# Optimization experiments

Measured on AMD Instinct MI355X. Metric: run time of the kernel, lower is better.

The kernel has to match this reference:

```python
import jax, jax.numpy as jnp
import numpy as np

N_NODES = 10000
N_EDGES = 320000
D = 128  # feature dim for edges, nodes, globals


def setup_inputs() -> dict:
    key = jax.random.key(0)
    ks = jax.random.split(key, 8)
    edges = jax.random.normal(ks[0], (N_EDGES, D), dtype=jnp.float32)
    nodes = jax.random.normal(ks[1], (N_NODES, D), dtype=jnp.float32)
    globals_ = jax.random.normal(ks[2], (D,), dtype=jnp.float32)
    receivers = jax.random.randint(ks[3], (N_EDGES,), 0, N_NODES, dtype=jnp.int32).astype(jnp.int64)
    senders = jax.random.randint(ks[4], (N_EDGES,), 0, N_NODES, dtype=jnp.int32).astype(jnp.int64)
    W1 = jax.random.normal(ks[5], (4 * D, 256), dtype=jnp.float32) * (1.0 / np.sqrt(4 * D))
    b1 = jnp.zeros((256,), dtype=jnp.float32)
    W2 = jax.random.normal(ks[6], (256, D), dtype=jnp.float32) * (1.0 / np.sqrt(256))
    b2 = jnp.zeros((D,), dtype=jnp.float32)
    return {"edges": edges, "nodes": nodes, "globals_": globals_,
            "receivers": receivers, "senders": senders,
            "W1": W1, "b1": b1, "W2": W2, "b2": b2}


def reference(edges, nodes, globals_, receivers, senders, W1, b1, W2, b2):
    # Gather adjacent node features to edges, broadcast globals, concat.
    recv_feats = nodes[receivers]                 # [E, D]
    send_feats = nodes[senders]                   # [E, D]
    glob_feats = jnp.broadcast_to(globals_, (edges.shape[0], globals_.shape[0]))  # [E, D]
    x = jnp.concatenate([edges, recv_feats, send_feats, glob_feats], axis=-1)     # [E, 4D]
    # Edge-update MLP: 4D -> 256 -> D with relu.
    h = jax.nn.relu(x @ W1 + b1)
    new_edges = h @ W2 + b2                       # [E, D]
    return new_edges
```

## Files before the change

kernel.cpp:

```cpp
#include <hip/hip_runtime.h>
#include <hip/hip_bf16.h>

#define D 128
#define NH 256
#define K1 384
#define BM 64
#define E_TOTAL 320000
#define NNODES 10000

typedef __attribute__((ext_vector_type(8))) short bf16x8;
typedef __attribute__((ext_vector_type(4))) float f32x4;

__device__ __forceinline__ unsigned short f2b(float f) {
  unsigned int u = __builtin_bit_cast(unsigned int, f);
  u += 0x7fffu + ((u >> 16) & 1u);
  return (unsigned short)(u >> 16);
}

__global__ void cast_nodes_kernel(const float* __restrict__ nodes,
                                  ushort* __restrict__ out) {
  int i = (blockIdx.x * 256 + threadIdx.x) * 4;
  float4 v = *(const float4*)(nodes + i);
  ushort4 b;
  b.x = f2b(v.x); b.y = f2b(v.y); b.z = f2b(v.z); b.w = f2b(v.w);
  *(ushort4*)(out + i) = b;
}

__global__ void pack_w1_kernel(const float* __restrict__ W1,
                               ushort* __restrict__ W1p) {
  int c = blockIdx.x * 256 + threadIdx.x;
  int nt = c / (12 * 64);
  int rem = c % (12 * 64);
  int ks = rem >> 6;
  int l = rem & 63;
  int col = nt * 16 + (l & 15);
  int k0 = ks * 32 + (l >> 4) * 8;
  ushort* dst = W1p + (size_t)c * 8;
  #pragma unroll
  for (int j = 0; j < 8; ++j)
    dst[j] = f2b(W1[(size_t)(k0 + j) * NH + col]);
}

__global__ void pack_w2_kernel(const float* __restrict__ W2,
                               ushort* __restrict__ W2p) {
  int c = blockIdx.x * 256 + threadIdx.x;
  int nt2 = c / (8 * 64);
  int rem = c % (8 * 64);
  int ks = rem >> 6;
  int l = rem & 63;
  int col = nt2 * 16 + (l & 15);
  int k0 = ks * 32 + (l >> 4) * 8;
  ushort* dst = W2p + (size_t)c * 8;
  #pragma unroll
  for (int j = 0; j < 8; ++j)
    dst[j] = f2b(W2[(size_t)(k0 + j) * D + col]);
}

__global__ void cvec_kernel(const float* __restrict__ W1,
                            const float* __restrict__ b1,
                            const float* __restrict__ g,
                            float* __restrict__ cvec) {
  int n = threadIdx.x;
  float acc = b1[n];
  for (int k = 0; k < D; ++k)
    acc += g[k] * W1[(size_t)(K1 + k) * NH + n];
  cvec[n] = acc;
}

__global__ __launch_bounds__(512, 6) void fused_kernel(
    const float* __restrict__ edges,
    const ushort* __restrict__ nodes_b,
    const int* __restrict__ receivers,
    const int* __restrict__ senders,
    const ushort* __restrict__ W1p,
    const float* __restrict__ cvec,
    const ushort* __restrict__ W2p,
    const float* __restrict__ b2,
    float* __restrict__ out) {
  __shared__ char Xs[BM * 768];
  char* Hs = Xs;

  const int ebase = blockIdx.x * BM;
  const int tid = threadIdx.x;

  const int gr0 = tid >> 4;
  const int gr1 = gr0 + 32;
  const int gc = (tid & 15) << 3;
  int idx_r0 = receivers[ebase + gr0];
  int idx_r1 = receivers[ebase + gr1];
  int idx_s0 = senders[ebase + gr0];
  int idx_s1 = senders[ebase + gr1];

  float4 ev[4];
  int er[4], ec[4];
  #pragma unroll
  for (int it = 0; it < 4; ++it) {
    int ch = tid + it * 512;
    er[it] = ch >> 5;
    ec[it] = (ch & 31) << 2;
    ev[it] = *(const float4*)(edges + (size_t)(ebase + er[it]) * D + ec[it]);
  }

  uint4 gv[4];
  gv[0] = *(const uint4*)(nodes_b + (size_t)idx_r0 * D + gc);
  gv[1] = *(const uint4*)(nodes_b + (size_t)idx_r1 * D + gc);
  gv[2] = *(const uint4*)(nodes_b + (size_t)idx_s0 * D + gc);
  gv[3] = *(const uint4*)(nodes_b + (size_t)idx_s1 * D + gc);

  #pragma unroll
  for (int it = 0; it < 4; ++it) {
    ushort4 b;
    b.x = f2b(ev[it].x); b.y = f2b(ev[it].y); b.z = f2b(ev[it].z); b.w = f2b(ev[it].w);
    *(ushort4*)(Xs + er[it] * 768 + ((ec[it] * 2) ^ ((er[it] & 7) << 4))) = b;
  }
  {
    int cR = (D + gc) * 2, cS = (2 * D + gc) * 2;
    *(uint4*)(Xs + gr0 * 768 + (cR ^ ((gr0 & 7) << 4))) = gv[0];
    *(uint4*)(Xs + gr1 * 768 + (cR ^ ((gr1 & 7) << 4))) = gv[1];
    *(uint4*)(Xs + gr0 * 768 + (cS ^ ((gr0 & 7) << 4))) = gv[2];
    *(uint4*)(Xs + gr1 * 768 + (cS ^ ((gr1 & 7) << 4))) = gv[3];
  }
  __syncthreads();

  const int lane = tid & 63;
  const int wave = tid >> 6;
  const int lr = lane & 15;
  const int kg = lane >> 4;
  const int wm3 = wave >> 1;
  const int wn3 = wave & 1;

  const ushort* w1base = W1p + (size_t)(wave * 2) * 12 * 512 + lane * 8;

  f32x4 acc[2][4] = {};
  bf16x8 aw[2][2];
  #pragma unroll
  for (int ht = 0; ht < 2; ++ht)
    aw[0][ht] = *(const bf16x8*)(w1base + (size_t)ht * 12 * 512);

  #pragma unroll
  for (int ks = 0; ks < 12; ++ks) {
    const int cur = ks & 1, nxt = cur ^ 1;
    if (ks < 11) {
      #pragma unroll
      for (int ht = 0; ht < 2; ++ht)
        aw[nxt][ht] = *(const bf16x8*)(w1base + (size_t)ht * 12 * 512 + (ks + 1) * 512);
    }
    const int k0 = ks * 32 + kg * 8;
    bf16x8 xb[4];
    #pragma unroll
    for (int et = 0; et < 4; ++et) {
      int row = et * 16 + lr;
      xb[et] = *(const bf16x8*)(Xs + row * 768 + ((k0 * 2) ^ ((row & 7) << 4)));
    }
    #pragma unroll
    for (int ht = 0; ht < 2; ++ht)
      #pragma unroll
      for (int et = 0; et < 4; ++et)
        acc[ht][et] = __builtin_amdgcn_mfma_f32_16x16x32_bf16(aw[cur][ht], xb[et], acc[ht][et], 0, 0, 0);
  }

  const ushort* w2base = W2p + (size_t)(wm3 * 2) * 8 * 512 + lane * 8;
  bf16x8 aw2[2][2];
  #pragma unroll
  for (int mt = 0; mt < 2; ++mt)
    aw2[0][mt] = *(const bf16x8*)(w2base + (size_t)mt * 8 * 512);
  float4 cva = *(const float4*)(cvec + wave * 32 + kg * 4);
  float4 cvb = *(const float4*)(cvec + wave * 32 + 16 + kg * 4);

  __syncthreads();

  #pragma unroll
  for (int ht = 0; ht < 2; ++ht) {
    const float4 cvq = ht ? cvb : cva;
    const int h0b = (wave * 32 + ht * 16 + kg * 4) * 2;
    #pragma unroll
    for (int et = 0; et < 4; ++et) {
      int e = et * 16 + lr;
      float v0 = acc[ht][et][0] + cvq.x;
      float v1 = acc[ht][et][1] + cvq.y;
      float v2 = acc[ht][et][2] + cvq.z;
      float v3 = acc[ht][et][3] + cvq.w;
      v0 = v0 > 0.f ? v0 : 0.f;
      v1 = v1 > 0.f ? v1 : 0.f;
      v2 = v2 > 0.f ? v2 : 0.f;
      v3 = v3 > 0.f ? v3 : 0.f;
      uint2 pk;
      pk.x = (unsigned)f2b(v0) | ((unsigned)f2b(v1) << 16);
      pk.y = (unsigned)f2b(v2) | ((unsigned)f2b(v3) << 16);
      *(uint2*)(Hs + e * 512 + (h0b ^ ((e & 7) << 4))) = pk;
    }
  }
  __syncthreads();

  float4 ba = *(const float4*)(b2 + wm3 * 32 + kg * 4);
  float4 bb2 = *(const float4*)(b2 + wm3 * 32 + 16 + kg * 4);
  f32x4 acc2[2][2] = {};
  #pragma unroll
  for (int ks = 0; ks < 8; ++ks) {
    const int cur = ks & 1, nxt = cur ^ 1;
    if (ks < 7) {
      #pragma unroll
      for (int mt = 0; mt < 2; ++mt)
        aw2[nxt][mt] = *(const bf16x8*)(w2base + (size_t)mt * 8 * 512 + (ks + 1) * 512);
    }
    const int k0 = ks * 32 + kg * 8;
    bf16x8 hb[2];
    #pragma unroll
    for (int et2 = 0; et2 < 2; ++et2) {
      int e = wn3 * 32 + et2 * 16 + lr;
      hb[et2] = *(const bf16x8*)(Hs + e * 512 + ((k0 * 2) ^ ((e & 7) << 4)));
    }
    #pragma unroll
    for (int mt = 0; mt < 2; ++mt)
      #pragma unroll
      for (int et2 = 0; et2 < 2; ++et2)
        acc2[mt][et2] = __builtin_amdgcn_mfma_f32_16x16x32_bf16(aw2[cur][mt], hb[et2], acc2[mt][et2], 0, 0, 0);
  }

  #pragma unroll
  for (int mt = 0; mt < 2; ++mt) {
    const float4 bq = mt ? bb2 : ba;
    const int c0 = wm3 * 32 + mt * 16 + kg * 4;
    #pragma unroll
    for (int et2 = 0; et2 < 2; ++et2) {
      int e = wn3 * 32 + et2 * 16 + lr;
      float4 o;
      o.x = acc2[mt][et2][0] + bq.x;
      o.y = acc2[mt][et2][1] + bq.y;
      o.z = acc2[mt][et2][2] + bq.z;
      o.w = acc2[mt][et2][3] + bq.w;
      *(float4*)(out + (size_t)(ebase + e) * D + c0) = o;
    }
  }
}

extern "C" void kernel_launch(void* const* d_in, const int* in_sizes, int n_in,
                              void* d_out, int out_size, void* d_ws, size_t ws_size,
                              hipStream_t stream) {
  const float* edges     = (const float*)d_in[0];
  const float* nodes     = (const float*)d_in[1];
  const float* globals_  = (const float*)d_in[2];
  const int*   receivers = (const int*)d_in[3];
  const int*   senders   = (const int*)d_in[4];
  const float* W1        = (const float*)d_in[5];
  const float* b1        = (const float*)d_in[6];
  const float* W2        = (const float*)d_in[7];
  const float* b2        = (const float*)d_in[8];
  float* out = (float*)d_out;

  char* ws = (char*)d_ws;
  ushort* nodes_b = (ushort*)ws;
  ushort* W1p     = (ushort*)(ws + 2560000);
  ushort* W2p     = (ushort*)(ws + 2560000 + 196608);
  float*  cvec    = (float*)(ws + 2560000 + 196608 + 65536);

  hipLaunchKernelGGL(cast_nodes_kernel, dim3(NNODES * D / 1024), dim3(256), 0, stream,
                     nodes, nodes_b);
  hipLaunchKernelGGL(pack_w1_kernel, dim3(48), dim3(256), 0, stream, W1, W1p);
  hipLaunchKernelGGL(pack_w2_kernel, dim3(16), dim3(256), 0, stream, W2, W2p);
  hipLaunchKernelGGL(cvec_kernel, dim3(1), dim3(256), 0, stream,
                     W1, b1, globals_, cvec);
  hipLaunchKernelGGL(fused_kernel, dim3(E_TOTAL / BM), dim3(512), 0, stream,
                     edges, nodes_b, receivers, senders, W1p, cvec, W2p, b2, out);
}
```

Before: 151.8 us.

## Precompute per-node first-layer projections and gather them instead of node features

Splits the first linear layer by linearity: node features are projected once per node through the receiver and sender slices of W1 into bf16 tables. The edge kernel gathers these 256-wide projections and adds them, plus the globals bias, into the hidden pre-activation. This cuts the edge GEMM K dimension from 384 to 128 and removes the node cast kernel. The cost is gathering 256-wide bf16 rows instead of 128-wide ones, extra bf16 rounding of the summed projections, a new pre-kernel, and lower declared occupancy.

```diff
diff --git a/kernel.cpp b/kernel.cpp
--- a/kernel.cpp
+++ b/kernel.cpp
@@ -3,7 +3,6 @@
 
 #define D 128
 #define NH 256
-#define K1 384
 #define BM 64
 #define E_TOTAL 320000
 #define NNODES 10000
@@ -16,26 +15,34 @@
   u += 0x7fffu + ((u >> 16) & 1u);
   return (unsigned short)(u >> 16);
 }
-
-__global__ void cast_nodes_kernel(const float* __restrict__ nodes,
-                                  ushort* __restrict__ out) {
-  int i = (blockIdx.x * 256 + threadIdx.x) * 4;
-  float4 v = *(const float4*)(nodes + i);
-  ushort4 b;
-  b.x = f2b(v.x); b.y = f2b(v.y); b.z = f2b(v.z); b.w = f2b(v.w);
-  *(ushort4*)(out + i) = b;
+__device__ __forceinline__ unsigned pk2(float a, float b) {
+  return (unsigned)f2b(a) | ((unsigned)f2b(b) << 16);
+}
+__device__ __forceinline__ uint4 pack8(float4 a, float4 b) {
+  uint4 r;
+  r.x = pk2(a.x, a.y); r.y = pk2(a.z, a.w);
+  r.z = pk2(b.x, b.y); r.w = pk2(b.z, b.w);
+  return r;
+}
+__device__ __forceinline__ float lo2f(unsigned u) {
+  return __builtin_bit_cast(float, u << 16);
+}
+__device__ __forceinline__ float hi2f(unsigned u) {
+  return __builtin_bit_cast(float, u & 0xffff0000u);
 }
 
 __global__ void pack_w1_kernel(const float* __restrict__ W1,
-                               ushort* __restrict__ W1p) {
+                               ushort* __restrict__ W1pk) {
   int c = blockIdx.x * 256 + threadIdx.x;
-  int nt = c / (12 * 64);
-  int rem = c % (12 * 64);
-  int ks = rem >> 6;
-  int l = rem & 63;
+  int s = c >> 12;
+  int rem = c & 4095;
+  int nt = rem >> 8;
+  int rem2 = rem & 255;
+  int ks = rem2 >> 6;
+  int l = rem2 & 63;
   int col = nt * 16 + (l & 15);
-  int k0 = ks * 32 + (l >> 4) * 8;
-  ushort* dst = W1p + (size_t)c * 8;
+  int k0 = s * 128 + ks * 32 + (l >> 4) * 8;
+  ushort* dst = W1pk + (size_t)c * 8;
   #pragma unroll
   for (int j = 0; j < 8; ++j)
     dst[j] = f2b(W1[(size_t)(k0 + j) * NH + col]);
@@ -63,62 +70,156 @@
   int n = threadIdx.x;
   float acc = b1[n];
   for (int k = 0; k < D; ++k)
-    acc += g[k] * W1[(size_t)(K1 + k) * NH + n];
+    acc += g[k] * W1[(size_t)(384 + k) * NH + n];
   cvec[n] = acc;
 }
 
-__global__ __launch_bounds__(512, 6) void fused_kernel(
+__global__ __launch_bounds__(512, 4) void nodeh_kernel(
+    const float* __restrict__ nodes,
+    const ushort* __restrict__ W1pk,
+    ushort* __restrict__ tblR,
+    ushort* __restrict__ tblS) {
+  __shared__ char Xn[BM * 256];
+  const int role = blockIdx.y;
+  ushort* __restrict__ tbl = role ? tblS : tblR;
+  const int nb = blockIdx.x * BM;
+  const int tid = threadIdx.x;
+
+  {
+    int row = tid >> 4;
+    int cc = (tid & 15) * 16;
+    #pragma unroll
+    for (int q = 0; q < 2; ++q) {
+      int r = row + q * 32;
+      int rg = nb + r; if (rg >= NNODES) rg = NNODES - 1;
+      const float* np = nodes + (size_t)rg * D + (tid & 15) * 8;
+      float4 u0 = *(const float4*)np;
+      float4 u1 = *(const float4*)(np + 4);
+      *(uint4*)(Xn + r * 256 + (cc ^ ((r & 7) << 4))) = pack8(u0, u1);
+    }
+  }
+  __syncthreads();
+
+  const int lane = tid & 63;
+  const int wave = tid >> 6;
+  const int lr = lane & 15;
+  const int kg = lane >> 4;
+
+  const ushort* wb = W1pk + (size_t)(1 + role) * 32768
+                   + (size_t)(wave * 2) * 2048 + lane * 8;
+  f32x4 acc[2][4] = {};
+  bf16x8 aw[2][2];
+  #pragma unroll
+  for (int ht = 0; ht < 2; ++ht)
+    aw[0][ht] = *(const bf16x8*)(wb + ht * 2048);
+
+  #pragma unroll
+  for (int ks = 0; ks < 4; ++ks) {
+    const int cur = ks & 1, nxt = cur ^ 1;
+    if (ks < 3) {
+      #pragma unroll
+      for (int ht = 0; ht < 2; ++ht)
+        aw[nxt][ht] = *(const bf16x8*)(wb + ht * 2048 + (ks + 1) * 512);
+    }
+    const int k0 = ks * 32 + kg * 8;
+    bf16x8 xb[4];
+    #pragma unroll
+    for (int et = 0; et < 4; ++et) {
+      int row = et * 16 + lr;
+      xb[et] = *(const bf16x8*)(Xn + row * 256 + ((k0 * 2) ^ ((row & 7) << 4)));
+    }
+    #pragma unroll
+    for (int ht = 0; ht < 2; ++ht)
+      #pragma unroll
+      for (int et = 0; et < 4; ++et)
+        acc[ht][et] = __builtin_amdgcn_mfma_f32_16x16x32_bf16(aw[cur][ht], xb[et], acc[ht][et], 0, 0, 0);
+  }
+
+  #pragma unroll
+  for (int ht = 0; ht < 2; ++ht) {
+    int h0 = wave * 32 + ht * 16 + kg * 4;
+    #pragma unroll
+    for (int et = 0; et < 4; ++et) {
+      int n = nb + et * 16 + lr;
+      if (n < NNODES) {
+        uint2 pk;
+        pk.x = pk2(acc[ht][et][0], acc[ht][et][1]);
+        pk.y = pk2(acc[ht][et][2], acc[ht][et][3]);
+        *(uint2*)(tbl + (size_t)n * NH + h0) = pk;
+      }
+    }
+  }
+}
+
+__global__ __launch_bounds__(512, 4) void fused_kernel(
     const float* __restrict__ edges,
-    const ushort* __restrict__ nodes_b,
     const int* __restrict__ receivers,
     const int* __restrict__ senders,
-    const ushort* __restrict__ W1p,
+    const ushort* __restrict__ W1pk,
+    const ushort* __restrict__ tblR,
+    const ushort* __restrict__ tblS,
     const float* __restrict__ cvec,
     const ushort* __restrict__ W2p,
     const float* __restrict__ b2,
     float* __restrict__ out) {
-  __shared__ char Xs[BM * 768];
-  char* Hs = Xs;
+  __shared__ char Xs[BM * 256];
+  __shared__ char Hp[BM * 512];
 
   const int ebase = blockIdx.x * BM;
   const int tid = threadIdx.x;
 
-  const int gr0 = tid >> 4;
-  const int gr1 = gr0 + 32;
-  const int gc = (tid & 15) << 3;
-  int idx_r0 = receivers[ebase + gr0];
-  int idx_r1 = receivers[ebase + gr1];
-  int idx_s0 = senders[ebase + gr0];
-  int idx_s1 = senders[ebase + gr1];
-
-  float4 ev[4];
-  int er[4], ec[4];
-  #pragma unroll
-  for (int it = 0; it < 4; ++it) {
-    int ch = tid + it * 512;
-    er[it] = ch >> 5;
-    ec[it] = (ch & 31) << 2;
-    ev[it] = *(const float4*)(edges + (size_t)(ebase + er[it]) * D + ec[it]);
-  }
-
-  uint4 gv[4];
-  gv[0] = *(const uint4*)(nodes_b + (size_t)idx_r0 * D + gc);
-  gv[1] = *(const uint4*)(nodes_b + (size_t)idx_r1 * D + gc);
-  gv[2] = *(const uint4*)(nodes_b + (size_t)idx_s0 * D + gc);
-  gv[3] = *(const uint4*)(nodes_b + (size_t)idx_s1 * D + gc);
-
-  #pragma unroll
-  for (int it = 0; it < 4; ++it) {
-    ushort4 b;
-    b.x = f2b(ev[it].x); b.y = f2b(ev[it].y); b.z = f2b(ev[it].z); b.w = f2b(ev[it].w);
-    *(ushort4*)(Xs + er[it] * 768 + ((ec[it] * 2) ^ ((er[it] & 7) << 4))) = b;
-  }
+  const int ge = tid >> 5;
+  const int gc0 = (tid & 31) * 8;
+  int idxR[4], idxS[4];
+  #pragma unroll
+  for (int j = 0; j < 4; ++j) {
+    idxR[j] = receivers[ebase + ge + j * 16];
+    idxS[j] = senders[ebase + ge + j * 16];
+  }
+
+  const int erow = tid >> 4;
+  const int ecc = (tid & 15) * 16;
+  float4 e0, e1, e2, e3;
   {
-    int cR = (D + gc) * 2, cS = (2 * D + gc) * 2;
-    *(uint4*)(Xs + gr0 * 768 + (cR ^ ((gr0 & 7) << 4))) = gv[0];
-    *(uint4*)(Xs + gr1 * 768 + (cR ^ ((gr1 & 7) << 4))) = gv[1];
-    *(uint4*)(Xs + gr0 * 768 + (cS ^ ((gr0 & 7) << 4))) = gv[2];
-    *(uint4*)(Xs + gr1 * 768 + (cS ^ ((gr1 & 7) << 4))) = gv[3];
+    const float* ep0 = edges + (size_t)(ebase + erow) * D + (tid & 15) * 8;
+    e0 = *(const float4*)ep0;
+    e1 = *(const float4*)(ep0 + 4);
+    const float* ep1 = edges + (size_t)(ebase + erow + 32) * D + (tid & 15) * 8;
+    e2 = *(const float4*)ep1;
+    e3 = *(const float4*)(ep1 + 4);
+  }
+
+  float4 cva = *(const float4*)(cvec + gc0);
+  float4 cvb = *(const float4*)(cvec + gc0 + 4);
+
+  uint4 gR[4], gS[4];
+  #pragma unroll
+  for (int j = 0; j < 4; ++j) {
+    gR[j] = *(const uint4*)(tblR + (size_t)idxR[j] * NH + gc0);
+    gS[j] = *(const uint4*)(tblS + (size_t)idxS[j] * NH + gc0);
+  }
+
+  *(uint4*)(Xs + erow * 256 + (ecc ^ ((erow & 7) << 4))) = pack8(e0, e1);
+  {
+    int r2 = erow + 32;
+    *(uint4*)(Xs + r2 * 256 + (ecc ^ ((r2 & 7) << 4))) = pack8(e2, e3);
+  }
+
+  #pragma unroll
+  for (int j = 0; j < 4; ++j) {
+    int e = ge + j * 16;
+    float s0 = lo2f(gR[j].x) + lo2f(gS[j].x) + cva.x;
+    float s1 = hi2f(gR[j].x) + hi2f(gS[j].x) + cva.y;
+    float s2 = lo2f(gR[j].y) + lo2f(gS[j].y) + cva.z;
+    float s3 = hi2f(gR[j].y) + hi2f(gS[j].y) + cva.w;
+    float s4 = lo2f(gR[j].z) + lo2f(gS[j].z) + cvb.x;
+    float s5 = hi2f(gR[j].z) + hi2f(gS[j].z) + cvb.y;
+    float s6 = lo2f(gR[j].w) + lo2f(gS[j].w) + cvb.z;
+    float s7 = hi2f(gR[j].w) + hi2f(gS[j].w) + cvb.w;
+    uint4 o;
+    o.x = pk2(s0, s1); o.y = pk2(s2, s3);
+    o.z = pk2(s4, s5); o.w = pk2(s6, s7);
+    *(uint4*)(Hp + e * 512 + ((gc0 * 2) ^ ((e & 7) << 4))) = o;
   }
   __syncthreads();
 
@@ -129,28 +230,27 @@
   const int wm3 = wave >> 1;
   const int wn3 = wave & 1;
 
-  const ushort* w1base = W1p + (size_t)(wave * 2) * 12 * 512 + lane * 8;
-
+  const ushort* w1base = W1pk + (size_t)(wave * 2) * 2048 + lane * 8;
   f32x4 acc[2][4] = {};
   bf16x8 aw[2][2];
   #pragma unroll
   for (int ht = 0; ht < 2; ++ht)
-    aw[0][ht] = *(const bf16x8*)(w1base + (size_t)ht * 12 * 512);
-
-  #pragma unroll
-  for (int ks = 0; ks < 12; ++ks) {
+    aw[0][ht] = *(const bf16x8*)(w1base + ht * 2048);
+
+  #pragma unroll
+  for (int ks = 0; ks < 4; ++ks) {
     const int cur = ks & 1, nxt = cur ^ 1;
-    if (ks < 11) {
+    if (ks < 3) {
       #pragma unroll
       for (int ht = 0; ht < 2; ++ht)
-        aw[nxt][ht] = *(const bf16x8*)(w1base + (size_t)ht * 12 * 512 + (ks + 1) * 512);
+        aw[nxt][ht] = *(const bf16x8*)(w1base + ht * 2048 + (ks + 1) * 512);
     }
     const int k0 = ks * 32 + kg * 8;
     bf16x8 xb[4];
     #pragma unroll
     for (int et = 0; et < 4; ++et) {
       int row = et * 16 + lr;
-      xb[et] = *(const bf16x8*)(Xs + row * 768 + ((k0 * 2) ^ ((row & 7) << 4)));
+      xb[et] = *(const bf16x8*)(Xs + row * 256 + ((k0 * 2) ^ ((row & 7) << 4)));
     }
     #pragma unroll
     for (int ht = 0; ht < 2; ++ht)
@@ -164,30 +264,27 @@
   #pragma unroll
   for (int mt = 0; mt < 2; ++mt)
     aw2[0][mt] = *(const bf16x8*)(w2base + (size_t)mt * 8 * 512);
-  float4 cva = *(const float4*)(cvec + wave * 32 + kg * 4);
-  float4 cvb = *(const float4*)(cvec + wave * 32 + 16 + kg * 4);
-
-  __syncthreads();
 
   #pragma unroll
   for (int ht = 0; ht < 2; ++ht) {
-    const float4 cvq = ht ? cvb : cva;
     const int h0b = (wave * 32 + ht * 16 + kg * 4) * 2;
     #pragma unroll
     for (int et = 0; et < 4; ++et) {
       int e = et * 16 + lr;
-      float v0 = acc[ht][et][0] + cvq.x;
-      float v1 = acc[ht][et][1] + cvq.y;
-      float v2 = acc[ht][et][2] + cvq.z;
-      float v3 = acc[ht][et][3] + cvq.w;
+      char* p = Hp + e * 512 + (h0b ^ ((e & 7) << 4));
+      uint2 hp = *(uint2*)p;
+      float v0 = acc[ht][et][0] + lo2f(hp.x);
+      float v1 = acc[ht][et][1] + hi2f(hp.x);
+      float v2 = acc[ht][et][2] + lo2f(hp.y);
+      float v3 = acc[ht][et][3] + hi2f(hp.y);
       v0 = v0 > 0.f ? v0 : 0.f;
       v1 = v1 > 0.f ? v1 : 0.f;
       v2 = v2 > 0.f ? v2 : 0.f;
       v3 = v3 > 0.f ? v3 : 0.f;
       uint2 pk;
-      pk.x = (unsigned)f2b(v0) | ((unsigned)f2b(v1) << 16);
-      pk.y = (unsigned)f2b(v2) | ((unsigned)f2b(v3) << 16);
-      *(uint2*)(Hs + e * 512 + (h0b ^ ((e & 7) << 4))) = pk;
+      pk.x = pk2(v0, v1);
+      pk.y = pk2(v2, v3);
+      *(uint2*)p = pk;
     }
   }
   __syncthreads();
@@ -208,7 +305,7 @@
     #pragma unroll
     for (int et2 = 0; et2 < 2; ++et2) {
       int e = wn3 * 32 + et2 * 16 + lr;
-      hb[et2] = *(const bf16x8*)(Hs + e * 512 + ((k0 * 2) ^ ((e & 7) << 4)));
+      hb[et2] = *(const bf16x8*)(Hp + e * 512 + ((k0 * 2) ^ ((e & 7) << 4)));
     }
     #pragma unroll
     for (int mt = 0; mt < 2; ++mt)
@@ -249,17 +346,18 @@
   float* out = (float*)d_out;
 
   char* ws = (char*)d_ws;
-  ushort* nodes_b = (ushort*)ws;
-  ushort* W1p     = (ushort*)(ws + 2560000);
-  ushort* W2p     = (ushort*)(ws + 2560000 + 196608);
-  float*  cvec    = (float*)(ws + 2560000 + 196608 + 65536);
-
-  hipLaunchKernelGGL(cast_nodes_kernel, dim3(NNODES * D / 1024), dim3(256), 0, stream,
-                     nodes, nodes_b);
-  hipLaunchKernelGGL(pack_w1_kernel, dim3(48), dim3(256), 0, stream, W1, W1p);
+  ushort* W1pk = (ushort*)ws;
+  ushort* W2p  = (ushort*)(ws + 196608);
+  float*  cvec = (float*)(ws + 262144);
+  ushort* tblR = (ushort*)(ws + 263168);
+  ushort* tblS = (ushort*)(ws + 5383168);
+
+  hipLaunchKernelGGL(pack_w1_kernel, dim3(48), dim3(256), 0, stream, W1, W1pk);
   hipLaunchKernelGGL(pack_w2_kernel, dim3(16), dim3(256), 0, stream, W2, W2p);
   hipLaunchKernelGGL(cvec_kernel, dim3(1), dim3(256), 0, stream,
                      W1, b1, globals_, cvec);
+  hipLaunchKernelGGL(nodeh_kernel, dim3((NNODES + BM - 1) / BM, 2), dim3(512), 0, stream,
+                     nodes, W1pk, tblR, tblS);
   hipLaunchKernelGGL(fused_kernel, dim3(E_TOTAL / BM), dim3(512), 0, stream,
-                     edges, nodes_b, receivers, senders, W1p, cvec, W2p, b2, out);
-}
+                     edges, receivers, senders, W1pk, tblR, tblS, cvec, W2p, b2, out);
+}
```

Measured after the change: 146.7 us. 1.03x faster.
